# Kernel optimization log

Measured on AMD Instinct MI355X. Metric: run time of the kernel, lower is better.

The kernel has to match this reference:

```python
import jax, jax.numpy as jnp
import numpy as np
import math

B, S, E, H, NL, OUT, VOCAB = 16, 512, 1024, 16, 6, 10, 16
D = E // H
PAD = VOCAB - 1
EPS = 1e-5


def _positional_encoding():
    # Faithful to the module: pe[:x.size(0)] indexes the BATCH dim of a
    # [B, S, E] tensor, yielding [B, 1, E] broadcast over sequence.
    pos = jnp.arange(B, dtype=jnp.float32)[:, None]            # [B,1]
    div = jnp.exp(jnp.arange(0, E, 2, dtype=jnp.float32) * (-math.log(10000.0) / E))
    pe = jnp.zeros((B, E), dtype=jnp.float32)
    pe = pe.at[:, 0::2].set(jnp.sin(pos * div))
    pe = pe.at[:, 1::2].set(jnp.cos(pos * div))
    return pe[:, None, :]                                      # [B,1,E]


def setup_inputs() -> dict:
    key = jax.random.key(0)
    ks = jax.random.split(key, 8)
    sc = 0.02
    return {
        "inputs": jax.random.randint(ks[0], (B, S), 0, PAD),   # no pad tokens
        "emb": jax.random.normal(ks[1], (VOCAB, E), jnp.float32) * sc,
        "wq": jax.random.normal(ks[2], (E, E), jnp.float32) * sc,
        "bq": jnp.zeros((E,), jnp.float32),
        "wk": jax.random.normal(ks[3], (E, E), jnp.float32) * sc,
        "bk": jnp.zeros((E,), jnp.float32),
        "wv": jax.random.normal(ks[4], (E, E), jnp.float32) * sc,
        "bv": jnp.zeros((E,), jnp.float32),
        "wfc": jax.random.normal(ks[5], (E, E), jnp.float32) * sc,
        "bfc": jnp.zeros((E,), jnp.float32),
        "gamma": jnp.ones((E,), jnp.float32),
        "beta": jnp.zeros((E,), jnp.float32),
        "wout": jax.random.normal(ks[6], (S * E, OUT), jnp.float32) * sc,
        "bout": jnp.zeros((OUT,), jnp.float32),
    }


def _layernorm(x, gamma, beta):
    mu = jnp.mean(x, axis=-1, keepdims=True)
    var = jnp.mean(jnp.square(x - mu), axis=-1, keepdims=True)
    return (x - mu) * jax.lax.rsqrt(var + EPS) * gamma + beta


def reference(inputs, emb, wq, bq, wk, bk, wv, bv, wfc, bfc, gamma, beta, wout, bout):
    x = emb[inputs]                                            # [B,S,E]
    x = x + (x + _positional_encoding())                       # x += pos_enc(x)
    mask = (inputs == PAD)                                     # [B,S] key-pad mask
    scale = 1.0 / math.sqrt(D)
    for _ in range(NL):  # same (shared) weights each iteration, as in source
        q = (x @ wq + bq).reshape(B, S, H, D).transpose(0, 2, 1, 3)
        k = (x @ wk + bk).reshape(B, S, H, D).transpose(0, 2, 1, 3)
        v = (x @ wv + bv).reshape(B, S, H, D).transpose(0, 2, 1, 3)
        att = jnp.einsum('bhqd,bhkd->bhqk', q, k) * scale      # [B,H,S,S]
        att = jnp.where(mask[:, None, None, :], -jnp.inf, att)
        att = jax.nn.softmax(att, axis=-1)
        o = jnp.einsum('bhqk,bhkd->bhqd', att, v)
        o = o.transpose(0, 2, 1, 3).reshape(B, S, E)
        x = _layernorm(o + x, gamma, beta)                     # dropout = eval identity
        x = _layernorm((x @ wfc + bfc) + x, gamma, beta)
    return x.reshape(B, -1) @ wout + bout                      # [B,OUT]
```

## Files before the change

kernel.cpp:

```cpp
#include <hip/hip_runtime.h>
#include <hip/hip_bf16.h>
#include <math.h>

#define B_   16
#define S_   512
#define E_   1024
#define H_   16
#define D_   64
#define NL_  6
#define OUT_ 10
#define M_   (B_*S_)

typedef short short8 __attribute__((ext_vector_type(8)));
typedef float f32x4 __attribute__((ext_vector_type(4)));
typedef int   int4v __attribute__((ext_vector_type(4)));
typedef unsigned short ushort4v __attribute__((ext_vector_type(4)));

typedef const __attribute__((address_space(1))) unsigned int* gas1_t;
typedef __attribute__((address_space(3))) unsigned int* las3_t;
#define GLD16(g,l) __builtin_amdgcn_global_load_lds((gas1_t)(g), (las3_t)(l), 16, 0, 0)
#define VMW(n) asm volatile("s_waitcnt vmcnt(" #n ")" ::: "memory")

static __device__ __forceinline__ float bf2f(unsigned short u){
  union { unsigned int i; float f; } v; v.i = ((unsigned int)u) << 16; return v.f;
}
static __device__ __forceinline__ unsigned short f2bf(float f){
  union { float f; unsigned int i; } v; v.f = f;
  unsigned int r = v.i + 0x7fffu + ((v.i >> 16) & 1u);
  return (unsigned short)(r >> 16);
}
static __device__ __forceinline__ f32x4 mfma16(short8 a, short8 b, f32x4 c){
  return __builtin_amdgcn_mfma_f32_16x16x32_bf16(a, b, c, 0, 0, 0);
}

__global__ __launch_bounds__(192)
void code_k(float* __restrict__ out, float code)
{
  int t = threadIdx.x;
  if (t < B_*OUT_) out[t] = code;
}

__global__ __launch_bounds__(256)
void transpose_k(const float* __restrict__ w0, const float* __restrict__ w1,
                 const float* __restrict__ w2, const float* __restrict__ w3,
                 unsigned short* __restrict__ wT)
{
  const float* w = blockIdx.z==0 ? w0 : blockIdx.z==1 ? w1 : blockIdx.z==2 ? w2 : w3;
  unsigned short* o = wT + (size_t)blockIdx.z * E_ * E_;
  __shared__ unsigned short tl[64][65];
  int n0 = blockIdx.x*64, k0 = blockIdx.y*64;
  int tx = threadIdx.x, ty = threadIdx.y;
  #pragma unroll
  for (int i = 0; i < 16; ++i)
    tl[ty + 4*i][tx] = f2bf(w[(size_t)(k0 + ty + 4*i)*E_ + n0 + tx]);
  __syncthreads();
  #pragma unroll
  for (int i = 0; i < 16; ++i)
    o[(size_t)(n0 + ty + 4*i)*E_ + k0 + tx] = tl[tx][ty + 4*i];
}

__global__ __launch_bounds__(256)
void embed_k(const int* __restrict__ tok, const float* __restrict__ emb,
             float* __restrict__ x, unsigned short* __restrict__ xb)
{
  int row = blockIdx.x;
  int b = row >> 9;
  int tk = tok[row];
  tk = tk < 0 ? 0 : (tk > 15 ? 15 : tk);
  int e0 = threadIdx.x * 4;
  const float c0 = -9.210340371976184f / (float)E_;
  f32x4 ev = *(const f32x4*)&emb[(size_t)tk * E_ + e0];
  f32x4 vv; ushort4v bb;
  #pragma unroll
  for (int i = 0; i < 4; ++i) {
    int e = e0 + i;
    float dv = expf((float)(e & ~1) * c0);
    float arg = (float)b * dv;
    float pe = (e & 1) ? cosf(arg) : sinf(arg);
    float v = 2.0f * ev[i] + pe;
    vv[i] = v; bb[i] = f2bf(v);
  }
  *(f32x4*)&x[(size_t)row*E_ + e0] = vv;
  *(ushort4v*)&xb[(size_t)row*E_ + e0] = bb;
}

template<int MODE>
__global__ __launch_bounds__(512, 2)
void gemm256_k(const unsigned short* __restrict__ A,
               const unsigned short* __restrict__ WT,
               const float* __restrict__ bq, const float* __restrict__ bk,
               const float* __restrict__ bv,
               unsigned short* __restrict__ out)
{
  extern __shared__ unsigned short SM2[];
  int mt = blockIdx.x, nt = blockIdx.y;
  int wsel = (MODE==0) ? (nt>>2) : 3;
  int ntl  = (MODE==0) ? (nt&3)  : nt;
  const unsigned short* Bp = WT + (MODE==0 ? (size_t)wsel*E_*E_ : (size_t)0) + (size_t)ntl*256*E_;
  const float* bias = (MODE==0) ? (wsel==0 ? bq : (wsel==1 ? bk : bv)) : bq;
  int m0 = mt*256;
  int tid = threadIdx.x, lane = tid&63, wid = tid>>6;
  int lr = lane&15, lk = lane>>4;
  int rl = tid>>3;
  int cs = (tid&7) ^ (rl&7);
  unsigned short* Ab0 = SM2;
  unsigned short* Ab1 = SM2 + 16384;
  unsigned short* Bb0 = SM2 + 32768;
  unsigned short* Bb1 = SM2 + 49152;

  f32x4 acc[16][2] = {};

  auto stA = [&](unsigned short* dst, int kt, int q) {
    GLD16(A + (size_t)(m0 + q*64 + rl)*E_ + kt*64 + cs*8, dst + ((q*512 + tid)<<3));
  };
  auto stB = [&](unsigned short* dst, int kt, int h) {
    GLD16(Bp + (size_t)(h*128 + rl)*E_ + kt*64 + cs*8,      dst + ((h*1024 + tid)<<3));
    GLD16(Bp + (size_t)(h*128 + 64 + rl)*E_ + kt*64 + cs*8, dst + ((h*1024 + 512 + tid)<<3));
  };

  stB(Bb0, 0, 0); stB(Bb0, 0, 1);
  stA(Ab0, 0, 0); stA(Ab0, 0, 1); stA(Ab0, 0, 2); stA(Ab0, 0, 3);

  int sw0 = (lk ^ (lr&7)) << 3;
  int sw1 = ((4+lk) ^ (lr&7)) << 3;
  for (int kt = 0; kt < 16; ++kt) {
    unsigned short* Ar = (kt & 1) ? Ab1 : Ab0;
    unsigned short* Br = (kt & 1) ? Bb1 : Bb0;
    unsigned short* An = (kt & 1) ? Ab0 : Ab1;
    unsigned short* Bn = (kt & 1) ? Bb0 : Bb1;
    bool more = (kt < 15);
    #pragma unroll
    for (int p = 0; p < 4; ++p) {
      if (more) {
        if (p == 0)      { stB(Bn, kt+1, 0); VMW(5); }
        else if (p == 1) { stB(Bn, kt+1, 1); VMW(6); }
        else if (p == 2) { stA(An, kt+1, 0); stA(An, kt+1, 1); VMW(7); }
        else             { stA(An, kt+1, 2); stA(An, kt+1, 3); VMW(8); }
      } else {
        if (p == 0)      VMW(3);
        else if (p == 1) VMW(2);
        else if (p == 2) VMW(1);
        else             VMW(0);
      }
      __builtin_amdgcn_s_barrier();
      short8 af[4][2], bfr[2][2];
      #pragma unroll
      for (int i = 0; i < 4; ++i) {
        int row = (p*4 + i)*16 + lr;
        af[i][0] = *(const short8*)&Ar[row*64 + sw0];
        af[i][1] = *(const short8*)&Ar[row*64 + sw1];
      }
      #pragma unroll
      for (int ni = 0; ni < 2; ++ni) {
        int row = wid*32 + ni*16 + lr;
        bfr[ni][0] = *(const short8*)&Br[row*64 + sw0];
        bfr[ni][1] = *(const short8*)&Br[row*64 + sw1];
      }
      __builtin_amdgcn_s_setprio(1);
      #pragma unroll
      for (int kk = 0; kk < 2; ++kk)
        #pragma unroll
        for (int i = 0; i < 4; ++i)
          #pragma unroll
          for (int ni = 0; ni < 2; ++ni)
            acc[p*4+i][ni] = mfma16(af[i][kk], bfr[ni][kk], acc[p*4+i][ni]);
      __builtin_amdgcn_s_setprio(0);
      __builtin_amdgcn_s_barrier();
    }
  }

  if (MODE == 1) {
    #pragma unroll
    for (int ni = 0; ni < 2; ++ni) {
      int n = ntl*256 + wid*32 + ni*16 + lr;
      float bv2 = bias[n];
      #pragma unroll
      for (int mi = 0; mi < 16; ++mi)
        #pragma unroll
        for (int j = 0; j < 4; ++j) {
          int m = m0 + mi*16 + lk*4 + j;
          out[(size_t)m*E_ + n] = f2bf(acc[mi][ni][j] + bv2);
        }
    }
  } else if (wsel < 2) {
    #pragma unroll
    for (int ni = 0; ni < 2; ++ni) {
      int n = ntl*256 + wid*32 + ni*16 + lr;
      float bv2 = bias[n];
      int h = n >> 6, d = n & 63;
      #pragma unroll
      for (int mi = 0; mi < 16; ++mi)
        #pragma unroll
        for (int j = 0; j < 4; ++j) {
          int m = m0 + mi*16 + lk*4 + j;
          int b = m >> 9, s = m & 511;
          out[(size_t)wsel*M_*E_ + (((size_t)(b*H_ + h)*S_ + s)*D_ + d)] =
            f2bf(acc[mi][ni][j] + bv2);
        }
    }
  } else {
    unsigned short* Cs = SM2;
    #pragma unroll
    for (int ni = 0; ni < 2; ++ni) {
      int nl = wid*32 + ni*16 + lr;
      float bv2 = bias[ntl*256 + nl];
      #pragma unroll
      for (int mi = 0; mi < 16; ++mi)
        #pragma unroll
        for (int j = 0; j < 4; ++j)
          Cs[nl*256 + mi*16 + lk*4 + j] = f2bf(acc[mi][ni][j] + bv2);
    }
    __syncthreads();
    int b = m0 >> 9, s0 = m0 & 511;
    #pragma unroll
    for (int j = 0; j < 16; ++j) {
      int id = j*512 + tid;
      int nl = id >> 5, mc = id & 31;
      int n = ntl*256 + nl;
      int h = n >> 6, d = n & 63;
      unsigned short* gp = out + (size_t)2*M_*E_ +
                           (((size_t)(b*H_ + h)*D_ + d)*S_ + s0 + mc*8);
      *(int4v*)gp = *(const int4v*)&Cs[nl*256 + mc*8];
    }
  }
}

__global__ __launch_bounds__(512, 4)
void attn_k(const unsigned short* __restrict__ Q, const unsigned short* __restrict__ K,
            const unsigned short* __restrict__ VT, unsigned short* __restrict__ O)
{
  extern __shared__ unsigned short SMEM[];
  int bid = blockIdx.x;
  int bh = bid & 255, qh = bid >> 8;
  int tid = threadIdx.x, lane = tid & 63, wid = tid >> 6;
  int lr = lane & 15, lk = lane >> 4;
  const unsigned short* Qb = Q + (size_t)bh * S_ * D_;
  const unsigned short* Kb = K + (size_t)bh * S_ * D_;
  const unsigned short* VTb = VT + (size_t)bh * S_ * D_;
  unsigned short* Pw = SMEM + 32768 + wid * 640;

  int kr  = tid >> 3, kc8 = tid & 7;
  int kcs = kc8 ^ (kr & 7);
  short8 qf[2][2];
  #pragma unroll
  for (int s = 0; s < 2; ++s) {
    int q0 = (qh*2 + s)*128 + wid*16;
    qf[s][0] = *(const short8*)(Qb + (size_t)(q0 + lr)*D_ + lk*8);
    qf[s][1] = *(const short8*)(Qb + (size_t)(q0 + lr)*D_ + 32 + lk*8);
  }
  {
    unsigned short* Kd = SMEM;
    #pragma unroll
    for (int j = 0; j < 2; ++j) {
      int idx = j*512 + tid;
      GLD16(Kb + (size_t)(kr + j*64)*D_ + kcs*8, &Kd[idx*8]);
    }
  }
  {
    unsigned short* Vd = SMEM + 16384;
    #pragma unroll
    for (int j = 0; j < 2; ++j) {
      int idx = j*512 + tid;
      int d = idx >> 4, c16 = idx & 15;
      int cds = c16 ^ (d & 15);
      GLD16(VTb + (size_t)d*S_ + cds*8, &Vd[idx*8]);
    }
  }
  __syncthreads();

  f32x4 oacc[2][4] = {};
  float plsum[2][4] = {{0.f,0.f,0.f,0.f},{0.f,0.f,0.f,0.f}};
  int cur = 0;
  for (int kt = 0; kt < 4; ++kt) {
    if (kt < 3) {
      unsigned short* Kd = SMEM + (cur^1)*8192;
      unsigned short* Vd = SMEM + 16384 + (cur^1)*8192;
      #pragma unroll
      for (int j = 0; j < 2; ++j) {
        int idx = j*512 + tid;
        int r = idx >> 3, c8 = idx & 7;
        GLD16(Kb + (size_t)((kt+1)*128 + r)*D_ + (c8 ^ (r & 7))*8, &Kd[idx*8]);
        int d = idx >> 4, c16 = idx & 15;
        GLD16(VTb + (size_t)d*S_ + (kt+1)*128 + (c16 ^ (d & 15))*8, &Vd[idx*8]);
      }
    }
    const unsigned short* Kl = SMEM + cur*8192;
    const unsigned short* Vl = SMEM + 16384 + cur*8192;
    #pragma unroll
    for (int s = 0; s < 2; ++s) {
      #pragma unroll
      for (int c = 0; c < 4; ++c) {
        f32x4 s0 = {}, s1 = {};
        {
          const unsigned short* kr0 = &Kl[((2*c)*16 + lr)*64];
          const unsigned short* kr1 = &Kl[((2*c+1)*16 + lr)*64];
          int a0 = ((lk     ^ (lr & 7)))*8;
          int a1 = (((4+lk) ^ (lr & 7)))*8;
          s0 = mfma16(qf[s][0], *(const short8*)(kr0 + a0), s0);
          s0 = mfma16(qf[s][1], *(const short8*)(kr0 + a1), s0);
          s1 = mfma16(qf[s][0], *(const short8*)(kr1 + a0), s1);
          s1 = mfma16(qf[s][1], *(const short8*)(kr1 + a1), s1);
        }
        #pragma unroll
        for (int j = 0; j < 4; ++j) {
          s0[j] = __expf(s0[j] * 0.125f);
          s1[j] = __expf(s1[j] * 0.125f);
          plsum[s][j] += s0[j] + s1[j];
        }
        #pragma unroll
        for (int j = 0; j < 4; ++j) {
          Pw[(lk*4 + j)*40 + lr]      = f2bf(s0[j]);
          Pw[(lk*4 + j)*40 + 16 + lr] = f2bf(s1[j]);
        }
        asm volatile("s_waitcnt lgkmcnt(0)" ::: "memory");
        short8 pf = *(const short8*)&Pw[lr*40 + lk*8];
        #pragma unroll
        for (int dt = 0; dt < 4; ++dt) {
          int drow = dt*16 + lr;
          short8 vf = *(const short8*)&Vl[drow*128 + (((c*4 + lk) ^ lr))*8];
          oacc[s][dt] = mfma16(pf, vf, oacc[s][dt]);
        }
      }
    }
    __syncthreads();
    cur ^= 1;
  }
  #pragma unroll
  for (int s = 0; s < 2; ++s) {
    float lsum[4];
    #pragma unroll
    for (int j = 0; j < 4; ++j) {
      float t = plsum[s][j];
      #pragma unroll
      for (int m = 1; m < 16; m <<= 1) t += __shfl_xor(t, m);
      lsum[j] = t;
    }
    int q0 = (qh*2 + s)*128 + wid*16;
    #pragma unroll
    for (int dt = 0; dt < 4; ++dt)
      #pragma unroll
      for (int j = 0; j < 4; ++j)
        O[(size_t)bh*S_*D_ + (size_t)(q0 + lk*4 + j)*D_ + dt*16 + lr] =
          f2bf(oacc[s][dt][j] / lsum[j]);
  }
}

template<bool PERM>
__global__ __launch_bounds__(256)
void ln_k(const unsigned short* __restrict__ g, float* __restrict__ x,
          unsigned short* __restrict__ xb,
          const float* __restrict__ gamma, const float* __restrict__ beta)
{
  int row = blockIdx.x;
  int tid = threadIdx.x;
  int e0 = tid * 4;
  ushort4v gu;
  if (PERM) {
    int b = row >> 9, s = row & 511;
    int h = e0 >> 6, d = e0 & 63;
    gu = *(const ushort4v*)&g[(((size_t)(b*H_ + h)*S_) + s)*D_ + d];
  } else {
    gu = *(const ushort4v*)&g[(size_t)row*E_ + e0];
  }
  f32x4 xv = *(const f32x4*)&x[(size_t)row*E_ + e0];
  f32x4 v;
  #pragma unroll
  for (int i = 0; i < 4; ++i) v[i] = bf2f(gu[i]) + xv[i];
  float sum = v[0]+v[1]+v[2]+v[3];
  float sq  = v[0]*v[0]+v[1]*v[1]+v[2]*v[2]+v[3]*v[3];
  #pragma unroll
  for (int m = 1; m < 64; m <<= 1) { sum += __shfl_xor(sum, m); sq += __shfl_xor(sq, m); }
  __shared__ float red[2][4];
  int lane = tid & 63, wid = tid >> 6;
  if (lane == 0) { red[0][wid] = sum; red[1][wid] = sq; }
  __syncthreads();
  float ts = red[0][0]+red[0][1]+red[0][2]+red[0][3];
  float tq = red[1][0]+red[1][1]+red[1][2]+red[1][3];
  float mu = ts * (1.0f/E_);
  float var = tq * (1.0f/E_) - mu*mu;
  float rsq = rsqrtf(var + 1e-5f);
  f32x4 y; ushort4v yb;
  #pragma unroll
  for (int i = 0; i < 4; ++i) {
    float t = (v[i]-mu)*rsq*gamma[e0+i] + beta[e0+i];
    y[i] = t; yb[i] = f2bf(t);
  }
  *(f32x4*)&x[(size_t)row*E_ + e0] = y;
  *(ushort4v*)&xb[(size_t)row*E_ + e0] = yb;
}

__global__ __launch_bounds__(256)
void outp_k(const float* __restrict__ x, const float* __restrict__ wout,
            float* __restrict__ part)
{
  int b = blockIdx.y;
  int chunk = blockIdx.x;
  int tid = threadIdx.x;
  float acc[OUT_] = {};
  const float* xr = x + (size_t)b * S_ * E_;
  for (int j = 0; j < 32; ++j) {
    int k = chunk*8192 + j*256 + tid;
    float xv = xr[k];
    const float* wr = wout + (size_t)k * OUT_;
    #pragma unroll
    for (int o = 0; o < OUT_; ++o) acc[o] += xv * wr[o];
  }
  #pragma unroll
  for (int o = 0; o < OUT_; ++o)
    #pragma unroll
    for (int m = 1; m < 64; m <<= 1) acc[o] += __shfl_xor(acc[o], m);
  __shared__ float red[4][OUT_];
  int lane = tid & 63, wid = tid >> 6;
  if (lane == 0) {
    #pragma unroll
    for (int o = 0; o < OUT_; ++o) red[wid][o] = acc[o];
  }
  __syncthreads();
  if (tid < OUT_) {
    float s = red[0][tid] + red[1][tid] + red[2][tid] + red[3][tid];
    part[((size_t)chunk*B_ + b)*OUT_ + tid] = s;
  }
}

__global__ __launch_bounds__(192)
void outred_k(const float* __restrict__ part, const float* __restrict__ bout,
              float* __restrict__ out)
{
  int t = threadIdx.x;
  if (t < B_*OUT_) {
    int b = t / OUT_, o = t % OUT_;
    float s = 0.f;
    for (int c = 0; c < 64; ++c) s += part[((size_t)c*B_ + b)*OUT_ + o];
    s += bout[o];
    out[t] = s;
  }
}

extern "C" void kernel_launch(void* const* d_in, const int* in_sizes, int n_in,
                              void* d_out, int out_size, void* d_ws, size_t ws_size,
                              hipStream_t stream)
{
  (void)out_size;
  float* outb = (float*)d_out;

  static const int expect[14] = {8192, 16384, 1048576, 1024, 1048576, 1024,
                                 1048576, 1024, 1048576, 1024, 1024, 1024,
                                 5242880, 10};
  if (n_in != 14) { code_k<<<dim3(1), dim3(192), 0, stream>>>(outb, 9000.0f); return; }
  for (int i = 0; i < 14; ++i)
    if (in_sizes[i] != expect[i]) {
      code_k<<<dim3(1), dim3(192), 0, stream>>>(outb, 5000.0f + 100.0f*i); return;
    }

  const int* tok = (const int*)d_in[0];
  const float* emb  = (const float*)d_in[1];
  const float* wq   = (const float*)d_in[2];
  const float* bq   = (const float*)d_in[3];
  const float* wk   = (const float*)d_in[4];
  const float* bk   = (const float*)d_in[5];
  const float* wv   = (const float*)d_in[6];
  const float* bv   = (const float*)d_in[7];
  const float* wfc  = (const float*)d_in[8];
  const float* bfc  = (const float*)d_in[9];
  const float* gam  = (const float*)d_in[10];
  const float* bet  = (const float*)d_in[11];
  const float* wout = (const float*)d_in[12];
  const float* bout = (const float*)d_in[13];

  char* ws = (char*)d_ws;
  size_t off = 0;
  unsigned short* wT = (unsigned short*)(ws + off); off += (size_t)4*E_*E_*2;
  float* x  = (float*)(ws + off);                   off += (size_t)M_*E_*4;
  unsigned short* xb = (unsigned short*)(ws + off); off += (size_t)M_*E_*2;
  unsigned short* qkvb = (unsigned short*)(ws + off); off += (size_t)3*M_*E_*2;
  unsigned short* gb = (unsigned short*)(ws + off); off += (size_t)M_*E_*2;
  float* part = (float*)(ws + off);                 off += (size_t)64*B_*OUT_*4;
  if (off > ws_size) { code_k<<<dim3(1), dim3(192), 0, stream>>>(outb, 9500.0f); return; }

  transpose_k<<<dim3(16,16,4), dim3(64,4), 0, stream>>>(wq, wk, wv, wfc, wT);
  embed_k<<<dim3(M_), dim3(256), 0, stream>>>(tok, emb, x, xb);
  unsigned short* qb = qkvb;
  unsigned short* kb = qkvb + (size_t)M_*E_;
  unsigned short* vb = qkvb + (size_t)2*M_*E_;
  for (int l = 0; l < NL_; ++l) {
    gemm256_k<0><<<dim3(32,12), dim3(512), 131072, stream>>>(xb, wT, bq, bk, bv, qkvb);
    attn_k<<<dim3(512), dim3(512), 75776, stream>>>(qb, kb, vb, gb);
    ln_k<true><<<dim3(M_), dim3(256), 0, stream>>>(gb, x, xb, gam, bet);
    gemm256_k<1><<<dim3(32,4), dim3(512), 131072, stream>>>(xb, wT + (size_t)3*E_*E_, bfc, bfc, bfc, gb);
    ln_k<false><<<dim3(M_), dim3(256), 0, stream>>>(gb, x, xb, gam, bet);
  }
  outp_k<<<dim3(64,B_), dim3(256), 0, stream>>>(x, wout, part);
  outred_k<<<dim3(1), dim3(192), 0, stream>>>(part, bout, outb);
}
```

Measured before the change: 1.075 ms.

## Shrink GEMM tile to 128x256 with triple-buffered LDS and coalesced epilogue

The QKV and FC GEMMs move from 256x256 to 128x256 tiles. This doubles the grid to 768 and 256 blocks, which fills more CUs. The double-buffered k-loop becomes a triple-buffered ring that prefetches two k-tiles ahead with adjusted vmcnt waits. The Q/K/row-major epilogues now stage results through padded LDS and write 16-byte vectors instead of scattered 2-byte stores. In exchange, LDS per block rises to 144KB, which limits residency to one block per CU, and each A tile reuses less of B.

```diff
diff --git a/kernel.cpp b/kernel.cpp
--- a/kernel.cpp
+++ b/kernel.cpp
@@ -98,63 +98,58 @@
   int ntl  = (MODE==0) ? (nt&3)  : nt;
   const unsigned short* Bp = WT + (MODE==0 ? (size_t)wsel*E_*E_ : (size_t)0) + (size_t)ntl*256*E_;
   const float* bias = (MODE==0) ? (wsel==0 ? bq : (wsel==1 ? bk : bv)) : bq;
-  int m0 = mt*256;
+  int m0 = mt*128;
   int tid = threadIdx.x, lane = tid&63, wid = tid>>6;
   int lr = lane&15, lk = lane>>4;
   int rl = tid>>3;
   int cs = (tid&7) ^ (rl&7);
-  unsigned short* Ab0 = SM2;
-  unsigned short* Ab1 = SM2 + 16384;
-  unsigned short* Bb0 = SM2 + 32768;
-  unsigned short* Bb1 = SM2 + 49152;
-
-  f32x4 acc[16][2] = {};
-
-  auto stA = [&](unsigned short* dst, int kt, int q) {
-    GLD16(A + (size_t)(m0 + q*64 + rl)*E_ + kt*64 + cs*8, dst + ((q*512 + tid)<<3));
+
+  unsigned short *a0 = SM2,          *a1 = SM2 + 8192,  *a2 = SM2 + 16384;
+  unsigned short *b0 = SM2 + 24576,  *b1 = SM2 + 40960, *b2 = SM2 + 57344;
+
+  f32x4 acc[8][2] = {};
+
+  auto stA = [&](unsigned short* dst, int kt) {
+    GLD16(A + (size_t)(m0 + rl)*E_ + kt*64 + cs*8,      dst + (tid<<3));
+    GLD16(A + (size_t)(m0 + 64 + rl)*E_ + kt*64 + cs*8, dst + ((512 + tid)<<3));
   };
-  auto stB = [&](unsigned short* dst, int kt, int h) {
-    GLD16(Bp + (size_t)(h*128 + rl)*E_ + kt*64 + cs*8,      dst + ((h*1024 + tid)<<3));
-    GLD16(Bp + (size_t)(h*128 + 64 + rl)*E_ + kt*64 + cs*8, dst + ((h*1024 + 512 + tid)<<3));
+  auto stB = [&](unsigned short* dst, int kt) {
+    GLD16(Bp + (size_t)(rl)*E_ + kt*64 + cs*8,       dst + (tid<<3));
+    GLD16(Bp + (size_t)(64 + rl)*E_ + kt*64 + cs*8,  dst + ((512 + tid)<<3));
+    GLD16(Bp + (size_t)(128 + rl)*E_ + kt*64 + cs*8, dst + ((1024 + tid)<<3));
+    GLD16(Bp + (size_t)(192 + rl)*E_ + kt*64 + cs*8, dst + ((1536 + tid)<<3));
   };
 
-  stB(Bb0, 0, 0); stB(Bb0, 0, 1);
-  stA(Ab0, 0, 0); stA(Ab0, 0, 1); stA(Ab0, 0, 2); stA(Ab0, 0, 3);
-
-  int sw0 = (lk ^ (lr&7)) << 3;
-  int sw1 = ((4+lk) ^ (lr&7)) << 3;
+  stB(b0, 0); stA(a0, 0);
+  stB(b1, 1); stA(a1, 1);
+
+  int sw0 = (lk ^ (lr&7)) * 8;
+  int sw1 = ((4+lk) ^ (lr&7)) * 8;
   for (int kt = 0; kt < 16; ++kt) {
-    unsigned short* Ar = (kt & 1) ? Ab1 : Ab0;
-    unsigned short* Br = (kt & 1) ? Bb1 : Bb0;
-    unsigned short* An = (kt & 1) ? Ab0 : Ab1;
-    unsigned short* Bn = (kt & 1) ? Bb0 : Bb1;
-    bool more = (kt < 15);
-    #pragma unroll
-    for (int p = 0; p < 4; ++p) {
-      if (more) {
-        if (p == 0)      { stB(Bn, kt+1, 0); VMW(5); }
-        else if (p == 1) { stB(Bn, kt+1, 1); VMW(6); }
-        else if (p == 2) { stA(An, kt+1, 0); stA(An, kt+1, 1); VMW(7); }
-        else             { stA(An, kt+1, 2); stA(An, kt+1, 3); VMW(8); }
+    #pragma unroll
+    for (int p = 0; p < 2; ++p) {
+      if (p == 0) {
+        if (kt < 14)      { stB(b2, kt+2); VMW(11); }
+        else if (kt == 14) VMW(7);
+        else               VMW(1);
       } else {
-        if (p == 0)      VMW(3);
-        else if (p == 1) VMW(2);
-        else if (p == 2) VMW(1);
-        else             VMW(0);
+        if (kt < 14)      { stA(a2, kt+2); VMW(12); }
+        else if (kt == 14) VMW(6);
+        else               VMW(0);
       }
       __builtin_amdgcn_s_barrier();
       short8 af[4][2], bfr[2][2];
       #pragma unroll
       for (int i = 0; i < 4; ++i) {
         int row = (p*4 + i)*16 + lr;
-        af[i][0] = *(const short8*)&Ar[row*64 + sw0];
-        af[i][1] = *(const short8*)&Ar[row*64 + sw1];
+        af[i][0] = *(const short8*)&a0[row*64 + sw0];
+        af[i][1] = *(const short8*)&a0[row*64 + sw1];
       }
       #pragma unroll
       for (int ni = 0; ni < 2; ++ni) {
         int row = wid*32 + ni*16 + lr;
-        bfr[ni][0] = *(const short8*)&Br[row*64 + sw0];
-        bfr[ni][1] = *(const short8*)&Br[row*64 + sw1];
+        bfr[ni][0] = *(const short8*)&b0[row*64 + sw0];
+        bfr[ni][1] = *(const short8*)&b0[row*64 + sw1];
       }
       __builtin_amdgcn_s_setprio(1);
       #pragma unroll
@@ -167,61 +162,61 @@
       __builtin_amdgcn_s_setprio(0);
       __builtin_amdgcn_s_barrier();
     }
-  }
-
-  if (MODE == 1) {
+    unsigned short* ta = a0; a0 = a1; a1 = a2; a2 = ta;
+    unsigned short* tb = b0; b0 = b1; b1 = b2; b2 = tb;
+  }
+
+  if (MODE == 1 || wsel < 2) {
+    unsigned short* Cs = SM2;
     #pragma unroll
     for (int ni = 0; ni < 2; ++ni) {
       int n = ntl*256 + wid*32 + ni*16 + lr;
       float bv2 = bias[n];
       #pragma unroll
-      for (int mi = 0; mi < 16; ++mi)
-        #pragma unroll
-        for (int j = 0; j < 4; ++j) {
-          int m = m0 + mi*16 + lk*4 + j;
-          out[(size_t)m*E_ + n] = f2bf(acc[mi][ni][j] + bv2);
-        }
-    }
-  } else if (wsel < 2) {
-    #pragma unroll
-    for (int ni = 0; ni < 2; ++ni) {
-      int n = ntl*256 + wid*32 + ni*16 + lr;
-      float bv2 = bias[n];
-      int h = n >> 6, d = n & 63;
-      #pragma unroll
-      for (int mi = 0; mi < 16; ++mi)
-        #pragma unroll
-        for (int j = 0; j < 4; ++j) {
-          int m = m0 + mi*16 + lk*4 + j;
-          int b = m >> 9, s = m & 511;
-          out[(size_t)wsel*M_*E_ + (((size_t)(b*H_ + h)*S_ + s)*D_ + d)] =
+      for (int mi = 0; mi < 8; ++mi)
+        #pragma unroll
+        for (int j = 0; j < 4; ++j)
+          Cs[(mi*16 + lk*4 + j)*272 + wid*32 + ni*16 + lr] =
             f2bf(acc[mi][ni][j] + bv2);
-        }
-    }
+    }
+    __syncthreads();
+    int r = tid >> 2, qd = tid & 3;
+    const unsigned short* sp = &Cs[r*272 + qd*64];
+    unsigned short* gp;
+    if (MODE == 1) {
+      gp = out + (size_t)(m0 + r)*E_ + ntl*256 + qd*64;
+    } else {
+      int m = m0 + r;
+      int b = m >> 9, s = m & 511;
+      int h = ntl*4 + qd;
+      gp = out + (size_t)wsel*M_*E_ + (((size_t)(b*H_ + h)*S_ + s)*D_);
+    }
+    #pragma unroll
+    for (int c = 0; c < 8; ++c)
+      *(int4v*)(gp + c*8) = *(const int4v*)(sp + c*8);
   } else {
-    unsigned short* Cs = SM2;
+    unsigned short* Ct = SM2;
     #pragma unroll
     for (int ni = 0; ni < 2; ++ni) {
       int nl = wid*32 + ni*16 + lr;
       float bv2 = bias[ntl*256 + nl];
       #pragma unroll
-      for (int mi = 0; mi < 16; ++mi)
+      for (int mi = 0; mi < 8; ++mi)
         #pragma unroll
         for (int j = 0; j < 4; ++j)
-          Cs[nl*256 + mi*16 + lk*4 + j] = f2bf(acc[mi][ni][j] + bv2);
+          Ct[nl*136 + mi*16 + lk*4 + j] = f2bf(acc[mi][ni][j] + bv2);
     }
     __syncthreads();
+    int nl = tid >> 1, half = tid & 1;
+    int n = ntl*256 + nl;
+    int h = n >> 6, d = n & 63;
     int b = m0 >> 9, s0 = m0 & 511;
-    #pragma unroll
-    for (int j = 0; j < 16; ++j) {
-      int id = j*512 + tid;
-      int nl = id >> 5, mc = id & 31;
-      int n = ntl*256 + nl;
-      int h = n >> 6, d = n & 63;
-      unsigned short* gp = out + (size_t)2*M_*E_ +
-                           (((size_t)(b*H_ + h)*D_ + d)*S_ + s0 + mc*8);
-      *(int4v*)gp = *(const int4v*)&Cs[nl*256 + mc*8];
-    }
+    unsigned short* gp = out + (size_t)2*M_*E_ +
+                         (((size_t)(b*H_ + h)*D_ + d)*S_ + s0 + half*64);
+    const unsigned short* sp = &Ct[nl*136 + half*64];
+    #pragma unroll
+    for (int c = 0; c < 8; ++c)
+      *(int4v*)(gp + c*8) = *(const int4v*)(sp + c*8);
   }
 }
 
@@ -483,10 +478,10 @@
   unsigned short* kb = qkvb + (size_t)M_*E_;
   unsigned short* vb = qkvb + (size_t)2*M_*E_;
   for (int l = 0; l < NL_; ++l) {
-    gemm256_k<0><<<dim3(32,12), dim3(512), 131072, stream>>>(xb, wT, bq, bk, bv, qkvb);
+    gemm256_k<0><<<dim3(64,12), dim3(512), 147456, stream>>>(xb, wT, bq, bk, bv, qkvb);
     attn_k<<<dim3(512), dim3(512), 75776, stream>>>(qb, kb, vb, gb);
     ln_k<true><<<dim3(M_), dim3(256), 0, stream>>>(gb, x, xb, gam, bet);
-    gemm256_k<1><<<dim3(32,4), dim3(512), 131072, stream>>>(xb, wT + (size_t)3*E_*E_, bfc, bfc, bfc, gb);
+    gemm256_k<1><<<dim3(64,4), dim3(512), 147456, stream>>>(xb, wT + (size_t)3*E_*E_, bfc, bfc, bfc, gb);
     ln_k<false><<<dim3(M_), dim3(256), 0, stream>>>(gb, x, xb, gam, bet);
   }
   outp_k<<<dim3(64,B_), dim3(256), 0, stream>>>(x, wout, part);
```

Result: faster. 1.038 ms (-3.4%).
